# Kernel tuning notes

Hardware: AMD Instinct MI355X
Metric: run time of the kernel (lower is better)

## Reference

```python
import jax, jax.numpy as jnp
import numpy as np

B, S, H, EMB, VOCAB, LABEL, NUM_LAYERS = 32, 512, 256, 256, 32000, 16, 3


def _before(x):  # shift right along seq dim, zero-pad front
    z = jnp.zeros_like(x[:, :1])
    return jnp.concatenate([z, x[:, :-1]], axis=1)


def _after(x):  # shift left along seq dim, zero-pad end
    z = jnp.zeros_like(x[:, :1])
    return jnp.concatenate([x[:, 1:], z], axis=1)


def setup_inputs() -> dict:
    key = jax.random.key(0)
    ks = jax.random.split(key, 12)
    p = lambda k, shape: (0.02 * jax.random.normal(k, shape)).astype(jnp.float32)
    return {
        "span_nodes": jnp.zeros((1,), jnp.int32),
        "bert_vec": jnp.zeros((1,), jnp.float32),
        "node_text": jax.random.randint(ks[0], (B, S), 0, VOCAB),
        "word_mask": jnp.ones((B, S), jnp.float32),
        "sent_mask": jnp.ones((1,), jnp.int32),
        "node_feature": jnp.zeros((1,), jnp.float32),
        "adj": jnp.zeros((1,), jnp.int32),
        # embedding + emb_proj
        "E": p(ks[1], (VOCAB, EMB)),
        "Wp": p(ks[2], (EMB, H)), "bp": jnp.zeros((H,), jnp.float32),
        # SCell: W(3H->7H, no bias), U(emb->7H, no bias), V(H->7H, bias)
        "Ws": p(ks[3], (3 * H, 7 * H)), "Us": p(ks[4], (EMB, 7 * H)),
        "Vs": p(ks[5], (H, 7 * H)), "bVs": jnp.zeros((7 * H,), jnp.float32),
        # GCell: W(H->2H, no bias), w(H->H, no bias), U(H->2H, bias), u(H->H, bias)
        "WgW": p(ks[6], (H, 2 * H)), "Wgw": p(ks[7], (H, H)),
        "UgU": p(ks[8], (H, 2 * H)), "bgU": jnp.zeros((2 * H,), jnp.float32),
        "ugu": p(ks[9], (H, H)), "bgu": jnp.zeros((H,), jnp.float32),
        # output head
        "Wo": p(ks[10], (H, LABEL)), "bo": jnp.zeros((LABEL,), jnp.float32),
    }


def _slstm(node_text, word_mask, E, Wp, bp, Ws, Us, Vs, bVs,
           WgW, Wgw, UgU, bgU, ugu, bgu, Wo, bo):
    mask = word_mask[..., None]                      # [B,S,1]
    emb = E[node_text]                               # [B,S,EMB]
    proj = (emb @ Wp + bp) * mask                    # [B,S,H] (dropout=identity in eval)
    h = proj
    c = proj
    g = h.mean(1)                                    # [B,H]
    c_g = c.mean(1)                                  # [B,H]
    xU = emb @ Us                                    # [B,S,7H] hoisted (constant per layer)
    neg = ((1.0 - word_mask) * 1e16)[..., None]      # [B,S,1]
    for _ in range(NUM_LAYERS):
        h = h * mask
        c = c * mask
        # SCell
        hcat = jnp.concatenate([_before(h), h, _after(h)], axis=-1)   # [B,S,3H]
        gates = hcat @ Ws + xU + (g @ Vs + bVs)[:, None, :]           # [B,S,7H]
        gi, gl, gr, gf, gs, go, gu = jnp.split(gates, 7, axis=-1)
        gu = jnp.tanh(gu)
        # sigmoid then softmax over the stacked-gate dim (note: o stays raw, as in source)
        stk = jax.nn.softmax(jax.nn.sigmoid(jnp.stack([gi, gl, gr, gf, gs], axis=-2)), axis=-2)
        gi, gl, gr, gf, gs = (stk[..., k, :] for k in range(5))
        new_c = _before(c) * gl + c * gf + gr * _after(c) + gs * c_g[:, None, :] + gi * gu
        new_h = go * jnp.tanh(new_c)
        # GCell (uses pre-update h, c)
        h_avg = h.mean(1)                                             # [B,H]
        fo = jax.nn.sigmoid(g @ WgW + h_avg @ UgU + bgU)              # [B,2H]
        f_g, o_g = jnp.split(fo, 2, axis=-1)
        f_w = jax.nn.sigmoid((g @ Wgw)[:, None, :] + h @ ugu + bgu) - neg   # [B,S,H]
        f_w = jax.nn.softmax(f_w, axis=1)
        new_c_g = f_g * c_g + (c * f_w).sum(1)
        new_g = o_g * jnp.tanh(new_c_g)
        h, c, g, c_g = new_h, new_c, new_g, new_c_g
    return (g @ Wo + bo, g.mean(0) @ Wo + bo)


def reference(span_nodes, bert_vec, node_text, word_mask, sent_mask, node_feature, adj,
              E, Wp, bp, Ws, Us, Vs, bVs, WgW, Wgw, UgU, bgU, ugu, bgu, Wo, bo):
    return _slstm(node_text, word_mask, E, Wp, bp, Ws, Us, Vs, bVs,
                  WgW, Wgw, UgU, bgU, ugu, bgu, Wo, bo)
```

## Files before the change

kernel.cpp:

```cpp
#include <hip/hip_runtime.h>
#include <math.h>

#define B_      32
#define S_      512
#define H_      256
#define EMB_    256
#define M_      (B_*S_)
#define N7_     1792
#define NG_     2048
#define NS_     2560
#define KA_     1024
#define LABEL_  16

#define BM 256
#define BN 256
#define BK 64
#define NT (KA_/BK)
#define EBM 64

typedef __bf16 bf16x8 __attribute__((ext_vector_type(8)));
typedef float  f32x4  __attribute__((ext_vector_type(4)));

__device__ __forceinline__ float sigf(float x){ return 1.f/(1.f+__expf(-x)); }

__device__ __forceinline__ unsigned short f2bf(float f){
    union { float f; unsigned int u; } v; v.f = f;
    unsigned int r = v.u + 0x7FFFu + ((v.u >> 16) & 1u);
    return (unsigned short)(r >> 16);
}
__device__ __forceinline__ float bf2f(unsigned short u){
    union { unsigned int i; float f; } v; v.i = ((unsigned int)u) << 16; return v.f;
}

__global__ void prep_waugT(const float* __restrict__ Ws, const float* __restrict__ Us,
                           const float* __restrict__ ugu, unsigned short* __restrict__ WaugT,
                           unsigned short* __restrict__ zpage){
    if(blockIdx.x == 0){ zpage[threadIdx.x] = 0; zpage[threadIdx.x + 256] = 0; }
    long idx = (long)blockIdx.x*256 + threadIdx.x;
    int j = (int)(idx >> 10), k = (int)(idx & 1023);
    int tg = j >> 7, rem = j & 127, p = rem >> 4, t = tg*16 + (rem & 15);
    float v = 0.f;
    if(p < 7){
        int col = p*256 + t;
        v = (k < 768) ? Ws[(long)k*N7_ + col] : Us[(long)(k-768)*N7_ + col];
    } else if(k >= 256 && k < 512){
        v = ugu[(k-256)*H_ + t];
    }
    WaugT[idx] = f2bf(v);
}

__global__ void prep_wpT(const float* __restrict__ Wp, unsigned short* __restrict__ WpT){
    int idx = blockIdx.x*256 + threadIdx.x;
    int j = idx >> 8, k = idx & 255;
    WpT[idx] = f2bf(Wp[k*H_ + j]);
}

__global__ void emb_cast(const int* __restrict__ idx, const float* __restrict__ E,
                         unsigned short* __restrict__ embbf){
    int i = blockIdx.x, t = threadIdx.x;
    embbf[(size_t)i*EMB_ + t] = f2bf(E[(size_t)idx[i]*EMB_ + t]);
}

__global__ __launch_bounds__(256, 2) void embed_mfma(
        const unsigned short* __restrict__ embbf, const unsigned short* __restrict__ WpT,
        const float* __restrict__ bp, const float* __restrict__ mask,
        unsigned short* __restrict__ h0b, float* __restrict__ c0){
    __shared__ unsigned short As[2][EBM*32];
    __shared__ unsigned short Bs[2][H_*32];
    int tid = threadIdx.x, w = tid>>6, l = tid&63, fr = l&15, fq = l>>4;
    int m0 = blockIdx.x * EBM;
    f32x4 acc[4][4];
    #pragma unroll
    for(int m=0;m<4;m++)
        #pragma unroll
        for(int n=0;n<4;n++) acc[m][n] = (f32x4){0.f,0.f,0.f,0.f};

    auto stage = [&](int buf, int kt){
        {
            int row = tid >> 2;
            int k0 = ((tid & 3) ^ ((row >> 1) & 3)) * 8;
            const unsigned short* src = embbf + (size_t)(m0+row)*EMB_ + kt + k0;
            __builtin_amdgcn_global_load_lds(
                (const __attribute__((address_space(1))) unsigned int*)src,
                (__attribute__((address_space(3))) unsigned int*)(&As[buf][w*512]),
                16, 0, 0);
        }
        #pragma unroll
        for(int q=0;q<4;q++){
            int v = q*256 + tid;
            int col = v >> 2;
            int k0 = ((v & 3) ^ ((col >> 1) & 3)) * 8;
            const unsigned short* src = WpT + (size_t)col*EMB_ + kt + k0;
            __builtin_amdgcn_global_load_lds(
                (const __attribute__((address_space(1))) unsigned int*)src,
                (__attribute__((address_space(3))) unsigned int*)(&Bs[buf][(q*256 + w*64)*8]),
                16, 0, 0);
        }
    };

    stage(0, 0);
    __syncthreads();
    int cur = 0;
    for(int step=0; step<EMB_/32; step++){
        if(step+1 < EMB_/32) stage(cur^1, (step+1)*32);
        bf16x8 bfv[4];
        #pragma unroll
        for(int n=0;n<4;n++){
            int colr = w*64 + n*16 + fr;
            int slot = fq ^ ((colr >> 1) & 3);
            bfv[n] = *(const bf16x8*)(&Bs[cur][colr*32 + slot*8]);
        }
        #pragma unroll
        for(int m=0;m<4;m++){
            int rowr = m*16 + fr;
            int slot = fq ^ ((rowr >> 1) & 3);
            bf16x8 af = *(const bf16x8*)(&As[cur][rowr*32 + slot*8]);
            #pragma unroll
            for(int n=0;n<4;n++)
                acc[m][n] = __builtin_amdgcn_mfma_f32_16x16x32_bf16(af, bfv[n], acc[m][n], 0,0,0);
        }
        __syncthreads();
        cur ^= 1;
    }
    #pragma unroll
    for(int m=0;m<4;m++){
        #pragma unroll
        for(int j=0;j<4;j++){
            int i = m0 + m*16 + fq*4 + j;
            float mk = mask[i];
            #pragma unroll
            for(int n=0;n<4;n++){
                int col = w*64 + n*16 + fr;
                float v = (acc[m][n][j] + bp[col]) * mk;
                h0b[(size_t)i*H_ + col] = f2bf(v);
                c0 [(size_t)i*H_ + col] = v;
            }
        }
    }
}

__global__ void reduce_mean_s(const unsigned short* __restrict__ h, float* __restrict__ outA,
                              float* __restrict__ outB){
    __shared__ float part[4][256];
    int b = blockIdx.x;
    int hh = threadIdx.x & 255, sg = threadIdx.x >> 8;
    float s = 0.f;
    long base = ((long)b*S_ + sg*128)*H_ + hh;
    for(int ss=0; ss<128; ss++) s += bf2f(h[base + (long)ss*H_]);
    part[sg][hh] = s;
    __syncthreads();
    if(threadIdx.x < 256){
        float t = (part[0][hh]+part[1][hh]+part[2][hh]+part[3][hh]) * (1.f/S_);
        outA[b*H_+hh] = t;
        if(outB) outB[b*H_+hh] = t;
    }
}

__global__ void small_gemm(const float* __restrict__ g, const float* __restrict__ havg,
                           const float* __restrict__ Vs, const float* __restrict__ bVs,
                           const float* __restrict__ Wgw, const float* __restrict__ bgu,
                           const float* __restrict__ WgW, const float* __restrict__ UgU,
                           const float* __restrict__ bgU, float* __restrict__ smalls){
    __shared__ float gs[256], hs[256];
    int b = blockIdx.y, t0 = threadIdx.x;
    gs[t0] = g[b*H_+t0];
    hs[t0] = havg[b*H_+t0];
    __syncthreads();
    int j = blockIdx.x*256 + t0;
    float acc;
    if(j < NG_){
        int tg = j >> 7, rem = j & 127, p = rem >> 4, t = tg*16 + (rem & 15);
        if(p < 7){
            int col = p*256 + t;
            acc = bVs[col];
            for(int k=0;k<H_;k++) acc += gs[k]*Vs[k*N7_+col];
        } else {
            acc = bgu[t];
            for(int k=0;k<H_;k++) acc += gs[k]*Wgw[k*H_+t];
        }
    } else {
        int jj = j - NG_;
        acc = bgU[jj];
        for(int k=0;k<H_;k++) acc += gs[k]*WgW[k*512+jj] + hs[k]*UgU[k*512+jj];
        acc = sigf(acc);
    }
    smalls[b*NS_+j] = acc;
}

__global__ __launch_bounds__(512, 2) void layer_mfma(
        const unsigned short* __restrict__ hbf, const unsigned short* __restrict__ embbf,
        const unsigned short* __restrict__ WaugT, const unsigned short* __restrict__ zpage,
        const float* __restrict__ c_old, const float* __restrict__ cg_old,
        const float* __restrict__ smalls, const float* __restrict__ mask,
        unsigned short* __restrict__ hbf_new, float* __restrict__ c_new,
        float* __restrict__ lpart, float* __restrict__ apart, float* __restrict__ hpart){
    __shared__ unsigned short As[2][BM*BK];
    __shared__ unsigned short Bs[2][BN*BK];
    __shared__ float red[8][16][3];
    int tid = threadIdx.x;
    int w = tid >> 6, l = tid & 63;
    int fr = l & 15, fq = l >> 4;
    int wr = w >> 1, wcl = w & 1;
    int m0 = blockIdx.x * BM;
    int n0 = blockIdx.y * BN;
    int b  = m0 >> 9;

    f32x4 acc[4][8];
    #pragma unroll
    for(int m=0;m<4;m++)
        #pragma unroll
        for(int n=0;n<8;n++) acc[m][n] = (f32x4){0.f,0.f,0.f,0.f};

    int rowc[2][2], k0a[2][2];
    #pragma unroll
    for(int p=0;p<2;p++)
        #pragma unroll
        for(int q=0;q<2;q++){
            int u = q*512 + tid;
            int row = p*128 + (u>>3);
            rowc[p][q] = row;
            k0a[p][q]  = ((u & 7) ^ (row & 7)) * 8;
        }
    const unsigned short* srcA[2][2];
    const unsigned short* srcB[2][2];
    #pragma unroll
    for(int hf=0;hf<2;hf++)
        #pragma unroll
        for(int q=0;q<2;q++){
            int u = q*512 + tid;
            int col = hf*128 + (u>>3);
            int k0 = ((u & 7) ^ (col & 7)) * 8;
            srcB[hf][q] = WaugT + (size_t)(n0 + col)*KA_ + k0;
        }
    auto setupA = [&](int r){
        #pragma unroll
        for(int p=0;p<2;p++)
            #pragma unroll
            for(int q=0;q<2;q++){
                int i = m0 + rowc[p][q];
                if(r < 3){
                    int si = (i & (S_-1)) + r - 1;
                    srcA[p][q] = ((unsigned)si < (unsigned)S_)
                               ? hbf + (size_t)(i + r - 1)*H_ + k0a[p][q]
                               : zpage + k0a[p][q];
                } else {
                    srcA[p][q] = embbf + (size_t)i*EMB_ + k0a[p][q];
                }
            }
    };
    auto advance = [&](){
        #pragma unroll
        for(int p=0;p<2;p++)
            #pragma unroll
            for(int q=0;q<2;q++){ srcA[p][q] += BK; srcB[p][q] += BK; }
    };
    auto stage_half = [&](int buf, int ph){
        if(ph < 2){
            #pragma unroll
            for(int q=0;q<2;q++)
                __builtin_amdgcn_global_load_lds(
                    (const __attribute__((address_space(1))) unsigned int*)srcA[ph][q],
                    (__attribute__((address_space(3))) unsigned int*)
                        (&As[buf][ph*8192 + (q*512 + w*64)*8]),
                    16, 0, 0);
        } else {
            int hf = ph - 2;
            #pragma unroll
            for(int q=0;q<2;q++)
                __builtin_amdgcn_global_load_lds(
                    (const __attribute__((address_space(1))) unsigned int*)srcB[hf][q],
                    (__attribute__((address_space(3))) unsigned int*)
                        (&Bs[buf][hf*8192 + (q*512 + w*64)*8]),
                    16, 0, 0);
        }
    };

    setupA(0);
    stage_half(0, 0); stage_half(0, 1); stage_half(0, 2); stage_half(0, 3);
    advance();

    bf16x8 afv[4];
    #pragma unroll 1
    for(int t=0; t<NT; ++t){
        int buf = t & 1;
        int st  = t + 1;
        #pragma unroll
        for(int p=0;p<4;p++){
            int ks = p >> 1, nh = p & 1;
            if(p == 0){
                asm volatile("s_waitcnt vmcnt(0)" ::: "memory");
                __builtin_amdgcn_s_barrier();
            }
            if(nh == 0){
                #pragma unroll
                for(int m=0;m<4;m++){
                    int row  = wr*64 + m*16 + fr;
                    int slot = (ks*4 + fq) ^ (row & 7);
                    afv[m] = *(const bf16x8*)(&As[buf][row*BK + slot*8]);
                }
            }
            bf16x8 bfv[4];
            #pragma unroll
            for(int nn=0;nn<4;nn++){
                int col  = wcl*128 + (nh*4+nn)*16 + fr;
                int slot = (ks*4 + fq) ^ (col & 7);
                bfv[nn] = *(const bf16x8*)(&Bs[buf][col*BK + slot*8]);
            }
            if(st < NT){
                if(p == 0 && (st & 3) == 0) setupA(st >> 2);
                stage_half(buf^1, p);
            }
            __builtin_amdgcn_s_barrier();
            asm volatile("s_waitcnt lgkmcnt(0)" ::: "memory");
            __builtin_amdgcn_sched_barrier(0);
            __builtin_amdgcn_s_setprio(1);
            #pragma unroll
            for(int m=0;m<4;m++)
                #pragma unroll
                for(int nn=0;nn<4;nn++)
                    acc[m][nh*4+nn] = __builtin_amdgcn_mfma_f32_16x16x32_bf16(
                                          afv[m], bfv[nn], acc[m][nh*4+nn], 0,0,0);
            __builtin_amdgcn_s_setprio(0);
            __builtin_amdgcn_sched_barrier(0);
            __builtin_amdgcn_s_barrier();
        }
        if(st < NT) advance();
    }

    int t = (n0 >> 3) + wcl*16 + fr;
    float sm[8];
    #pragma unroll
    for(int n=0;n<8;n++) sm[n] = smalls[b*NS_ + n0 + wcl*128 + n*16 + fr];
    float cgv = cg_old[b*H_ + t];
    float lsum = 0.f, asum = 0.f, hsum = 0.f;
    #pragma unroll
    for(int m=0;m<4;m++){
        #pragma unroll
        for(int j=0;j<4;j++){
            int i = m0 + wr*64 + m*16 + fq*4 + j;
            int s = i & (S_-1);
            float gv[8];
            #pragma unroll
            for(int n=0;n<8;n++) gv[n] = acc[m][n][j] + sm[n];
            float ei=__expf(sigf(gv[0])), el=__expf(sigf(gv[1])), er=__expf(sigf(gv[2]));
            float ef=__expf(sigf(gv[3])), es=__expf(sigf(gv[4]));
            float inv = 1.f/(ei+el+er+ef+es);
            float c0v = c_old[(size_t)i*H_ + t];
            float cbv = (s>0)      ? c_old[(size_t)(i-1)*H_ + t] : 0.f;
            float cav = (s<S_-1)   ? c_old[(size_t)(i+1)*H_ + t] : 0.f;
            float tu = tanhf(gv[6]);
            float nc = (cbv*el + c0v*ef + er*cav + es*cgv + ei*tu)*inv;
            float nh2 = gv[5]*tanhf(nc);
            float mk = mask[i];
            float ncm = nc*mk, nhm = nh2*mk;
            c_new [(size_t)i*H_ + t] = ncm;
            hbf_new[(size_t)i*H_ + t] = f2bf(nhm);
            float e = __expf(sigf(gv[7]) - (1.f - mk)*1e16f);
            lsum += e;
            asum += e*c0v;
            hsum += nhm;
        }
    }
    #pragma unroll
    for(int off=16; off<64; off<<=1){
        lsum += __shfl_xor(lsum, off);
        asum += __shfl_xor(asum, off);
        hsum += __shfl_xor(hsum, off);
    }
    if(l < 16){ red[w][l][0]=lsum; red[w][l][1]=asum; red[w][l][2]=hsum; }
    __syncthreads();
    if(tid < 32){
        int wc2 = tid >> 4, fr2 = tid & 15;
        float L = 0.f, A = 0.f, Hh = 0.f;
        #pragma unroll
        for(int k=0;k<4;k++){
            L  += red[2*k + wc2][fr2][0];
            A  += red[2*k + wc2][fr2][1];
            Hh += red[2*k + wc2][fr2][2];
        }
        int tt = (n0 >> 3) + wc2*16 + fr2;
        int by = blockIdx.x;
        lpart[by*H_ + tt] = L;
        apart[by*H_ + tt] = A;
        hpart[by*H_ + tt] = Hh;
    }
}

__global__ void gcell2x(const float* __restrict__ lpart, const float* __restrict__ apart,
                        const float* __restrict__ hpart, const float* __restrict__ cg_old,
                        const float* __restrict__ smalls,
                        float* __restrict__ g_new, float* __restrict__ cg_new,
                        float* __restrict__ havg_out){
    int b = blockIdx.x, t = threadIdx.x;
    float L = 0.f, A = 0.f, Hs = 0.f;
    for(int ci=0; ci<2; ci++){
        int by = b*2 + ci;
        L  += lpart[by*H_ + t];
        A  += apart[by*H_ + t];
        Hs += hpart[by*H_ + t];
    }
    float fg = smalls[b*NS_ + NG_ + t];
    float og = smalls[b*NS_ + NG_ + 256 + t];
    float ncg = fg*cg_old[b*H_+t] + A/L;
    g_new[b*H_+t]    = og*tanhf(ncg);
    cg_new[b*H_+t]   = ncg;
    havg_out[b*H_+t] = Hs * (1.f/S_);
}

__global__ void outk(const float* __restrict__ g, const float* __restrict__ Wo,
                     const float* __restrict__ bo, float* __restrict__ out){
    __shared__ float o1[B_*LABEL_];
    int t = threadIdx.x;
    if(t < B_*LABEL_){
        int b = t/LABEL_, j = t%LABEL_;
        float acc = bo[j];
        for(int k=0;k<H_;k++) acc += g[b*H_+k]*Wo[k*LABEL_+j];
        o1[t] = acc;
        out[t] = acc;
    }
    __syncthreads();
    if(t < LABEL_){
        float s = 0.f;
        for(int b=0;b<B_;b++) s += o1[b*LABEL_+t];
        out[B_*LABEL_+t] = s*(1.f/B_);
    }
}

extern "C" void kernel_launch(void* const* d_in, const int* in_sizes, int n_in,
                              void* d_out, int out_size, void* d_ws, size_t ws_size,
                              hipStream_t stream){
    const int*   node_text = (const int*)  d_in[2];
    const float* word_mask = (const float*)d_in[3];
    const float* E   = (const float*)d_in[7];
    const float* Wp  = (const float*)d_in[8];
    const float* bp  = (const float*)d_in[9];
    const float* Ws  = (const float*)d_in[10];
    const float* Us  = (const float*)d_in[11];
    const float* Vs  = (const float*)d_in[12];
    const float* bVs = (const float*)d_in[13];
    const float* WgW = (const float*)d_in[14];
    const float* Wgw = (const float*)d_in[15];
    const float* UgU = (const float*)d_in[16];
    const float* bgU = (const float*)d_in[17];
    const float* ugu = (const float*)d_in[18];
    const float* bgu = (const float*)d_in[19];
    const float* Wo  = (const float*)d_in[20];
    const float* bo  = (const float*)d_in[21];

    float* w = (float*)d_ws;
    size_t off = 0;
    auto alloc = [&](size_t nfloats){ float* p = w + off; off += nfloats; return p; };
    unsigned short* WaugT = (unsigned short*)alloc((size_t)NG_*KA_/2);
    unsigned short* zpage = (unsigned short*)alloc(256);
    unsigned short* WpT   = (unsigned short*)alloc((size_t)H_*EMB_/2);
    unsigned short* embbf = (unsigned short*)alloc((size_t)M_*EMB_/2);
    unsigned short* hbf[2] = { (unsigned short*)alloc((size_t)M_*H_/2),
                               (unsigned short*)alloc((size_t)M_*H_/2) };
    float* cb[2]  = { alloc((size_t)M_*H_), alloc((size_t)M_*H_) };
    float* lpart  = alloc((size_t)(M_/BM)*H_);
    float* apart  = alloc((size_t)(M_/BM)*H_);
    float* hpart  = alloc((size_t)(M_/BM)*H_);
    float* gb[2]  = { alloc(B_*H_), alloc(B_*H_) };
    float* cgb[2] = { alloc(B_*H_), alloc(B_*H_) };
    float* havg   = alloc(B_*H_);
    float* smalls = alloc((size_t)B_*NS_);

    prep_waugT<<<(NG_*KA_)/256, 256, 0, stream>>>(Ws, Us, ugu, WaugT, zpage);
    prep_wpT<<<(H_*EMB_)/256, 256, 0, stream>>>(Wp, WpT);
    emb_cast<<<M_, 256, 0, stream>>>(node_text, E, embbf);
    embed_mfma<<<M_/EBM, 256, 0, stream>>>(embbf, WpT, bp, word_mask, hbf[0], cb[0]);
    reduce_mean_s<<<B_, 1024, 0, stream>>>(hbf[0], gb[0], cgb[0]);

    int cur = 0;
    for(int layer=0; layer<3; layer++){
        int nxt = cur ^ 1;
        const float* havg_in = (layer == 0) ? gb[0] : havg;
        small_gemm<<<dim3(NS_/256, B_), 256, 0, stream>>>(gb[cur], havg_in, Vs, bVs,
                                                          Wgw, bgu, WgW, UgU, bgU, smalls);
        layer_mfma<<<dim3(M_/BM, NG_/BN), 512, 0, stream>>>(hbf[cur], embbf, WaugT, zpage,
                                                            cb[cur], cgb[cur], smalls, word_mask,
                                                            hbf[nxt], cb[nxt],
                                                            lpart, apart, hpart);
        gcell2x<<<B_, 256, 0, stream>>>(lpart, apart, hpart, cgb[cur], smalls,
                                        gb[nxt], cgb[nxt], havg);
        cur = nxt;
    }
    outk<<<1, 512, 0, stream>>>(gb[cur], Wo, bo, (float*)d_out);
}
```

Before: 374.2 us.

## Merge prep kernels with 8-wide bf16 stores and deepen layer GEMM prefetch

Three preprocessing kernels (weight transpose/cast, Wp transpose, embedding gather/cast) become one launch where each thread writes eight bf16 values as a single vector store. In the main layer GEMM, the first quarter of the next K-tile is issued before waiting, with a partial vmcnt(2) wait instead of a full drain, so loads overlap the barrier. One sched_barrier is dropped. The weight transpose reads stay strided per thread, so memory coalescing may get worse.

```diff
diff --git a/kernel.cpp b/kernel.cpp
--- a/kernel.cpp
+++ b/kernel.cpp
@@ -20,6 +20,7 @@
 
 typedef __bf16 bf16x8 __attribute__((ext_vector_type(8)));
 typedef float  f32x4  __attribute__((ext_vector_type(4)));
+typedef unsigned short us8 __attribute__((ext_vector_type(8)));
 
 __device__ __forceinline__ float sigf(float x){ return 1.f/(1.f+__expf(-x)); }
 
@@ -32,33 +33,56 @@
     union { unsigned int i; float f; } v; v.i = ((unsigned int)u) << 16; return v.f;
 }
 
-__global__ void prep_waugT(const float* __restrict__ Ws, const float* __restrict__ Us,
-                           const float* __restrict__ ugu, unsigned short* __restrict__ WaugT,
-                           unsigned short* __restrict__ zpage){
-    if(blockIdx.x == 0){ zpage[threadIdx.x] = 0; zpage[threadIdx.x + 256] = 0; }
-    long idx = (long)blockIdx.x*256 + threadIdx.x;
-    int j = (int)(idx >> 10), k = (int)(idx & 1023);
-    int tg = j >> 7, rem = j & 127, p = rem >> 4, t = tg*16 + (rem & 15);
-    float v = 0.f;
-    if(p < 7){
-        int col = p*256 + t;
-        v = (k < 768) ? Ws[(long)k*N7_ + col] : Us[(long)(k-768)*N7_ + col];
-    } else if(k >= 256 && k < 512){
-        v = ugu[(k-256)*H_ + t];
-    }
-    WaugT[idx] = f2bf(v);
-}
-
-__global__ void prep_wpT(const float* __restrict__ Wp, unsigned short* __restrict__ WpT){
-    int idx = blockIdx.x*256 + threadIdx.x;
-    int j = idx >> 8, k = idx & 255;
-    WpT[idx] = f2bf(Wp[k*H_ + j]);
-}
-
-__global__ void emb_cast(const int* __restrict__ idx, const float* __restrict__ E,
-                         unsigned short* __restrict__ embbf){
-    int i = blockIdx.x, t = threadIdx.x;
-    embbf[(size_t)i*EMB_ + t] = f2bf(E[(size_t)idx[i]*EMB_ + t]);
+#define WAUG_TH (NG_*KA_/8)
+#define WPT_TH  (H_*EMB_/8)
+#define EMB_TH  (M_*EMB_/8)
+#define PREP_TH (WAUG_TH + WPT_TH + EMB_TH)
+
+__global__ void prep_all(const float* __restrict__ Ws, const float* __restrict__ Us,
+                         const float* __restrict__ ugu, const float* __restrict__ Wp,
+                         const int* __restrict__ idx, const float* __restrict__ E,
+                         unsigned short* __restrict__ WaugT, unsigned short* __restrict__ WpT,
+                         unsigned short* __restrict__ embbf, unsigned short* __restrict__ zpage){
+    long u = (long)blockIdx.x*256 + threadIdx.x;
+    if(u < 512) zpage[u] = 0;
+    if(u < WAUG_TH){
+        int j  = (int)(u >> 7);
+        int kc = ((int)u & 127) * 8;
+        int tg = j >> 7, rem = j & 127, p = rem >> 4, t = tg*16 + (rem & 15);
+        us8 o;
+        if(p < 7){
+            int col = p*256 + t;
+            #pragma unroll
+            for(int x=0;x<8;x++){
+                int k = kc + x;
+                float v = (k < 768) ? Ws[(long)k*N7_ + col] : Us[(long)(k-768)*N7_ + col];
+                o[x] = f2bf(v);
+            }
+        } else {
+            #pragma unroll
+            for(int x=0;x<8;x++){
+                int k = kc + x;
+                float v = (k >= 256 && k < 512) ? ugu[(k-256)*H_ + t] : 0.f;
+                o[x] = f2bf(v);
+            }
+        }
+        *(us8*)&WaugT[(long)j*KA_ + kc] = o;
+    } else if(u < WAUG_TH + WPT_TH){
+        long v = u - WAUG_TH;
+        int j = (int)(v >> 5), kc = ((int)v & 31)*8;
+        us8 o;
+        #pragma unroll
+        for(int x=0;x<8;x++) o[x] = f2bf(Wp[(long)(kc+x)*H_ + j]);
+        *(us8*)&WpT[(long)j*EMB_ + kc] = o;
+    } else if(u < PREP_TH){
+        long v = u - WAUG_TH - WPT_TH;
+        int i = (int)(v >> 5), kc = ((int)v & 31)*8;
+        const float* src = E + (size_t)idx[i]*EMB_ + kc;
+        us8 o;
+        #pragma unroll
+        for(int x=0;x<8;x++) o[x] = f2bf(src[x]);
+        *(us8*)&embbf[(size_t)i*EMB_ + kc] = o;
+    }
 }
 
 __global__ __launch_bounds__(256, 2) void embed_mfma(
@@ -284,13 +308,17 @@
     for(int t=0; t<NT; ++t){
         int buf = t & 1;
         int st  = t + 1;
+        if(st < NT){
+            if((st & 3) == 0) setupA(st >> 2);
+            stage_half(buf^1, 0);
+            asm volatile("s_waitcnt vmcnt(2)" ::: "memory");
+        } else {
+            asm volatile("s_waitcnt vmcnt(0)" ::: "memory");
+        }
+        __builtin_amdgcn_s_barrier();
         #pragma unroll
         for(int p=0;p<4;p++){
             int ks = p >> 1, nh = p & 1;
-            if(p == 0){
-                asm volatile("s_waitcnt vmcnt(0)" ::: "memory");
-                __builtin_amdgcn_s_barrier();
-            }
             if(nh == 0){
                 #pragma unroll
                 for(int m=0;m<4;m++){
@@ -306,10 +334,7 @@
                 int slot = (ks*4 + fq) ^ (col & 7);
                 bfv[nn] = *(const bf16x8*)(&Bs[buf][col*BK + slot*8]);
             }
-            if(st < NT){
-                if(p == 0 && (st & 3) == 0) setupA(st >> 2);
-                stage_half(buf^1, p);
-            }
+            if(p < 3 && st < NT) stage_half(buf^1, p+1);
             __builtin_amdgcn_s_barrier();
             asm volatile("s_waitcnt lgkmcnt(0)" ::: "memory");
             __builtin_amdgcn_sched_barrier(0);
@@ -321,7 +346,6 @@
                     acc[m][nh*4+nn] = __builtin_amdgcn_mfma_f32_16x16x32_bf16(
                                           afv[m], bfv[nn], acc[m][nh*4+nn], 0,0,0);
             __builtin_amdgcn_s_setprio(0);
-            __builtin_amdgcn_sched_barrier(0);
             __builtin_amdgcn_s_barrier();
         }
         if(st < NT) advance();
@@ -465,9 +489,8 @@
     float* havg   = alloc(B_*H_);
     float* smalls = alloc((size_t)B_*NS_);
 
-    prep_waugT<<<(NG_*KA_)/256, 256, 0, stream>>>(Ws, Us, ugu, WaugT, zpage);
-    prep_wpT<<<(H_*EMB_)/256, 256, 0, stream>>>(Wp, WpT);
-    emb_cast<<<M_, 256, 0, stream>>>(node_text, E, embbf);
+    prep_all<<<(PREP_TH + 255)/256, 256, 0, stream>>>(Ws, Us, ugu, Wp, node_text, E,
+                                                      WaugT, WpT, embbf, zpage);
     embed_mfma<<<M_/EBM, 256, 0, stream>>>(embbf, WpT, bp, word_mask, hbf[0], cb[0]);
     reduce_mean_s<<<B_, 1024, 0, stream>>>(hbf[0], gb[0], cgb[0]);
 
```

Result: slower. 383.5 us (+2.5%).
